# Performance work log

Hardware: AMD Instinct MI355X
Metric: run time of the kernel (lower is better)

Reference implementation:

```python
import jax, jax.numpy as jnp
import numpy as np

B, H, SQ, SK, D, INT, F = 1, 32, 2048, 2048, 128, 128, 32
THOLD = 0.5


def _mlp(x, W1, b1, W2, b2, W3, b3):
    # x: [b,h,s,d]; W*: [h,out,in] (torch Linear layout), y = x @ W^T + b, per head
    h = jax.nn.silu(jnp.einsum('bhsd,hid->bhsi', x, W1) + b1[None, :, None, :])
    h = jax.nn.silu(jnp.einsum('bhsi,hji->bhsj', h, W2) + b2[None, :, None, :])
    return jnp.einsum('bhsj,hfj->bhsf', h, W3) + b3[None, :, None, :]


def setup_inputs() -> dict:
    key = jax.random.key(0)
    ks = jax.random.split(key, 16)
    sc = 0.05  # small init so tanh stays in its linear-ish range
    inp = {
        'K': jax.random.normal(ks[0], (B, H, SK, D), jnp.float32),
        'Q': jax.random.normal(ks[1], (B, H, SQ, D), jnp.float32),
        'Wk1': jax.random.normal(ks[2], (H, INT, D), jnp.float32) * sc,
        'bk1': jax.random.normal(ks[3], (H, INT), jnp.float32) * sc,
        'Wk2': jax.random.normal(ks[4], (H, INT, INT), jnp.float32) * sc,
        'bk2': jax.random.normal(ks[5], (H, INT), jnp.float32) * sc,
        'Wk3': jax.random.normal(ks[6], (H, F, INT), jnp.float32) * sc,
        'bk3': jax.random.normal(ks[7], (H, F), jnp.float32) * sc,
        'Wq1': jax.random.normal(ks[8], (H, INT, D), jnp.float32) * sc,
        'bq1': jax.random.normal(ks[9], (H, INT), jnp.float32) * sc,
        'Wq2': jax.random.normal(ks[10], (H, INT, INT), jnp.float32) * sc,
        'bq2': jax.random.normal(ks[11], (H, INT), jnp.float32) * sc,
        'Wq3': jax.random.normal(ks[12], (H, F, INT), jnp.float32) * sc,
        'bq3': jax.random.normal(ks[13], (H, F), jnp.float32) * sc,
    }
    return inp


def reference(K, Q, Wk1, bk1, Wk2, bk2, Wk3, bk3, Wq1, bq1, Wq2, bq2, Wq3, bq3):
    # soft (hard=False) path of USA.forward
    Kl = jnp.tanh(_mlp(K, Wk1, bk1, Wk2, bk2, Wk3, bk3))  # [b,h,sk,F]
    Ql = jnp.tanh(_mlp(Q, Wq1, bq1, Wq2, bq2, Wq3, bq3))  # [b,h,sq,F]
    scores = jnp.einsum('bhtf,bhsf->bhts', Ql, Kl)        # [b,h,sq,sk]
    sq, sk = Q.shape[2], K.shape[2]
    causal = jnp.tril(jnp.ones((sq, sk), dtype=bool), k=sk - sq)
    mask_val = jnp.asarray(jnp.finfo(scores.dtype).min, scores.dtype)
    scores = jnp.where(causal[None, None], scores, mask_val)
    return jax.nn.sigmoid(scores - THOLD)
```

## Files before the change

kernel.cpp:

```cpp
#include <hip/hip_runtime.h>

#define NH  32
#define SEQ 2048
#define DIM 128
#define FD  32

typedef short          short8 __attribute__((ext_vector_type(8)));
typedef float          f32x4  __attribute__((ext_vector_type(4)));
typedef unsigned short u16x4  __attribute__((ext_vector_type(4)));

static __device__ __forceinline__ unsigned short f2bf(float f) {
    unsigned int u = __builtin_bit_cast(unsigned int, f);
    u += 0x7fffu + ((u >> 16) & 1u);
    return (unsigned short)(u >> 16);
}
static __device__ __forceinline__ float fexp(float x) {
    return __builtin_amdgcn_exp2f(x * 1.44269504088896f);
}
static __device__ __forceinline__ float sigm(float x) {
    return __builtin_amdgcn_rcpf(1.0f + fexp(-x));
}
static __device__ __forceinline__ float silu_f(float x) { return x * sigm(x); }
static __device__ __forceinline__ float tanh_f(float x) {
    return 1.0f - 2.0f * __builtin_amdgcn_rcpf(fexp(2.0f * x) + 1.0f);
}

static __device__ __forceinline__ void stage_mat(const float* __restrict__ src,
                                                 unsigned short* dst, int rows) {
    int t = threadIdx.x;
    int nit = rows >> 2;
    for (int it = 0; it < nit; ++it) {
        int row = it * 4 + (t >> 5);
        int c0  = (t & 31) * 4;
        f32x4 v = *(const f32x4*)(src + row * 128 + c0);
        u16x4 p;
        p[0] = f2bf(v[0]); p[1] = f2bf(v[1]); p[2] = f2bf(v[2]); p[3] = f2bf(v[3]);
        int base = row * 128 + (c0 ^ ((row & 7) << 3));
        *(u16x4*)(&dst[base]) = p;
    }
}

template <int OT, int ACT, bool TOGLOB>
static __device__ __forceinline__ void mlp_layer(
    unsigned short* act, const unsigned short* w_lds,
    const float* __restrict__ bias, unsigned short* __restrict__ gout) {
    int lane = threadIdx.x & 63;
    int wid  = threadIdx.x >> 6;
    int kb   = (lane >> 4) * 8;

    short8 a[2][4];
#pragma unroll
    for (int rt = 0; rt < 2; ++rt) {
        int row = wid * 32 + rt * 16 + (lane & 15);
        int sw  = (row & 7) << 3;
#pragma unroll
        for (int ks = 0; ks < 4; ++ks)
            a[rt][ks] = *(const short8*)(&act[row * 128 + ((ks * 32 + kb) ^ sw)]);
    }
    __syncthreads();
#pragma unroll
    for (int ot = 0; ot < OT; ++ot) {
        int wrow = ot * 16 + (lane & 15);
        int sw   = (wrow & 7) << 3;
        short8 b[4];
#pragma unroll
        for (int ks = 0; ks < 4; ++ks)
            b[ks] = *(const short8*)(&w_lds[wrow * 128 + ((ks * 32 + kb) ^ sw)]);
        f32x4 acc0 = {0.f, 0.f, 0.f, 0.f};
        f32x4 acc1 = {0.f, 0.f, 0.f, 0.f};
#pragma unroll
        for (int ks = 0; ks < 4; ++ks) {
            acc0 = __builtin_amdgcn_mfma_f32_16x16x32_bf16(a[0][ks], b[ks], acc0, 0, 0, 0);
            acc1 = __builtin_amdgcn_mfma_f32_16x16x32_bf16(a[1][ks], b[ks], acc1, 0, 0, 0);
        }
        float bv = bias[ot * 16 + (lane & 15)];
#pragma unroll
        for (int rt = 0; rt < 2; ++rt) {
            f32x4 acc = rt ? acc1 : acc0;
#pragma unroll
            for (int r = 0; r < 4; ++r) {
                float y = acc[r] + bv;
                float v = (ACT == 0) ? silu_f(y) : tanh_f(y);
                int orow = wid * 32 + rt * 16 + (lane >> 4) * 4 + r;
                int ocol = ot * 16 + (lane & 15);
                if (TOGLOB)
                    gout[orow * FD + ocol] = f2bf(v);
                else
                    act[orow * 128 + (ocol ^ ((orow & 7) << 3))] = f2bf(v);
            }
        }
    }
}

__global__ __launch_bounds__(128) void mlp_kernel(
    const float* __restrict__ K,  const float* __restrict__ Q,
    const float* __restrict__ Wk1, const float* __restrict__ bk1,
    const float* __restrict__ Wk2, const float* __restrict__ bk2,
    const float* __restrict__ Wk3, const float* __restrict__ bk3,
    const float* __restrict__ Wq1, const float* __restrict__ bq1,
    const float* __restrict__ Wq2, const float* __restrict__ bq2,
    const float* __restrict__ Wq3, const float* __restrict__ bq3,
    unsigned short* __restrict__ Kl, unsigned short* __restrict__ Ql) {
    __shared__ unsigned short xb[64 * 128];
    __shared__ unsigned short wb[128 * 128];
    int bid = blockIdx.x;
    int tb  = bid & 31;
    int h   = (bid >> 5) & 31;
    int src = bid >> 10;

    const float* X  = src ? Q : K;
    const float* W1 = (src ? Wq1 : Wk1) + h * (128 * 128);
    const float* B1 = (src ? bq1 : bk1) + h * 128;
    const float* W2 = (src ? Wq2 : Wk2) + h * (128 * 128);
    const float* B2 = (src ? bq2 : bk2) + h * 128;
    const float* W3 = (src ? Wq3 : Wk3) + h * (FD * 128);
    const float* B3 = (src ? bq3 : bk3) + h * FD;
    unsigned short* gout = (src ? Ql : Kl) + ((size_t)h * SEQ + (size_t)tb * 64) * FD;
    const float* xs = X + ((size_t)h * SEQ + (size_t)tb * 64) * DIM;

    stage_mat(xs, xb, 64);
    stage_mat(W1, wb, 128);
    __syncthreads();
    mlp_layer<8, 0, false>(xb, wb, B1, nullptr);
    __syncthreads();
    stage_mat(W2, wb, 128);
    __syncthreads();
    mlp_layer<8, 0, false>(xb, wb, B2, nullptr);
    __syncthreads();
    stage_mat(W3, wb, 32);
    __syncthreads();
    mlp_layer<2, 1, true>(xb, wb, B3, gout);
}

__global__ __launch_bounds__(256) void score_kernel(
    const unsigned short* __restrict__ Ql, const unsigned short* __restrict__ Kl,
    float* __restrict__ out) {
    int bid = blockIdx.x;
    int h   = bid >> 8;
    int tr  = (bid >> 4) & 15;
    int tc  = bid & 15;
    int tq0 = tr * 128, tk0 = tc * 128;
    int tid = threadIdx.x;
    float* ob = out + (size_t)h * SEQ * SEQ;

    if (tc > tr) {
        f32x4 z = {0.f, 0.f, 0.f, 0.f};
        for (int it = 0; it < 16; ++it) {
            int row = tq0 + it * 8 + (tid >> 5);
            int c0  = tk0 + (tid & 31) * 4;
            *(f32x4*)(ob + (size_t)row * SEQ + c0) = z;
        }
        return;
    }
    bool diag = (tc == tr);
    __shared__ float sb[4][32 * 68];
    int lane = tid & 63;
    int wid  = tid >> 6;
    int tqw  = tq0 + (wid >> 1) * 64;
    int tkw  = tk0 + (wid & 1) * 64;
    int kb   = (lane >> 4) * 8;

    short8 aq[4], bk[4];
#pragma unroll
    for (int i = 0; i < 4; ++i) {
        aq[i] = *(const short8*)(Ql + ((size_t)h * SEQ + tqw + i * 16 + (lane & 15)) * FD + kb);
        bk[i] = *(const short8*)(Kl + ((size_t)h * SEQ + tkw + i * 16 + (lane & 15)) * FD + kb);
    }
    float* my = sb[wid];
#pragma unroll
    for (int half = 0; half < 2; ++half) {
#pragma unroll
        for (int rt2 = 0; rt2 < 2; ++rt2) {
            int rt = half * 2 + rt2;
#pragma unroll
            for (int ct = 0; ct < 4; ++ct) {
                f32x4 acc = {0.f, 0.f, 0.f, 0.f};
                acc = __builtin_amdgcn_mfma_f32_16x16x32_bf16(aq[rt], bk[ct], acc, 0, 0, 0);
#pragma unroll
                for (int r = 0; r < 4; ++r) {
                    int row = rt2 * 16 + (lane >> 4) * 4 + r;
                    int col = ct * 16 + (lane & 15);
                    float o = sigm(acc[r] - 0.5f);
                    if (diag && (tkw + col) > (tqw + half * 32 + row)) o = 0.0f;
                    my[row * 68 + col] = o;
                }
            }
        }
#pragma unroll
        for (int it = 0; it < 4; ++it) {
            int row = it * 8 + (lane >> 3);
            int c0  = (lane & 7) * 8;
            f32x4 v0 = *(const f32x4*)(&my[row * 68 + c0]);
            f32x4 v1 = *(const f32x4*)(&my[row * 68 + c0 + 4]);
            float* dst = ob + (size_t)(tqw + half * 32 + row) * SEQ + tkw + c0;
            *(f32x4*)dst       = v0;
            *(f32x4*)(dst + 4) = v1;
        }
    }
}

extern "C" void kernel_launch(void* const* d_in, const int* in_sizes, int n_in,
                              void* d_out, int out_size, void* d_ws, size_t ws_size,
                              hipStream_t stream) {
    const float* K   = (const float*)d_in[0];
    const float* Q   = (const float*)d_in[1];
    const float* Wk1 = (const float*)d_in[2];
    const float* bk1 = (const float*)d_in[3];
    const float* Wk2 = (const float*)d_in[4];
    const float* bk2 = (const float*)d_in[5];
    const float* Wk3 = (const float*)d_in[6];
    const float* bk3 = (const float*)d_in[7];
    const float* Wq1 = (const float*)d_in[8];
    const float* bq1 = (const float*)d_in[9];
    const float* Wq2 = (const float*)d_in[10];
    const float* bq2 = (const float*)d_in[11];
    const float* Wq3 = (const float*)d_in[12];
    const float* bq3 = (const float*)d_in[13];

    unsigned short* Kl = (unsigned short*)d_ws;
    unsigned short* Ql = Kl + (size_t)NH * SEQ * FD;

    mlp_kernel<<<dim3(2 * NH * (SEQ / 64)), dim3(128), 0, stream>>>(
        K, Q, Wk1, bk1, Wk2, bk2, Wk3, bk3, Wq1, bq1, Wq2, bq2, Wq3, bq3, Kl, Ql);

    score_kernel<<<dim3(NH * 16 * 16), dim3(256), 0, stream>>>(
        Ql, Kl, (float*)d_out);
}
```

Baseline: 173.6 us.

## Pre-convert MLP weights to bf16 once and read them directly from global memory

Adds a prep kernel that converts all MLP weights to a packed bf16 image in the workspace. The MLP kernel then reads weight fragments straight from global/L2 instead of staging them in LDS, loads the input tile directly into registers, and reorders block indices so blocks of the same head share cached weights. Layer 3 output is staged in LDS and written with vector stores, and the score kernel uses nontemporal stores for its large output. This removes repeated per-block fp32-to-bf16 weight conversion and LDS staging barriers, at the cost of an extra launch and more global weight traffic per block.

```diff
diff --git a/kernel.cpp b/kernel.cpp
--- a/kernel.cpp
+++ b/kernel.cpp
@@ -8,6 +8,7 @@
 typedef short          short8 __attribute__((ext_vector_type(8)));
 typedef float          f32x4  __attribute__((ext_vector_type(4)));
 typedef unsigned short u16x4  __attribute__((ext_vector_type(4)));
+typedef unsigned short u16x8  __attribute__((ext_vector_type(8)));
 
 static __device__ __forceinline__ unsigned short f2bf(float f) {
     unsigned int u = __builtin_bit_cast(unsigned int, f);
@@ -24,48 +25,72 @@
 static __device__ __forceinline__ float tanh_f(float x) {
     return 1.0f - 2.0f * __builtin_amdgcn_rcpf(fexp(2.0f * x) + 1.0f);
 }
-
-static __device__ __forceinline__ void stage_mat(const float* __restrict__ src,
-                                                 unsigned short* dst, int rows) {
-    int t = threadIdx.x;
-    int nit = rows >> 2;
-    for (int it = 0; it < nit; ++it) {
-        int row = it * 4 + (t >> 5);
-        int c0  = (t & 31) * 4;
-        f32x4 v = *(const f32x4*)(src + row * 128 + c0);
-        u16x4 p;
-        p[0] = f2bf(v[0]); p[1] = f2bf(v[1]); p[2] = f2bf(v[2]); p[3] = f2bf(v[3]);
-        int base = row * 128 + (c0 ^ ((row & 7) << 3));
-        *(u16x4*)(&dst[base]) = p;
-    }
-}
-
-template <int OT, int ACT, bool TOGLOB>
-static __device__ __forceinline__ void mlp_layer(
-    unsigned short* act, const unsigned short* w_lds,
-    const float* __restrict__ bias, unsigned short* __restrict__ gout) {
-    int lane = threadIdx.x & 63;
-    int wid  = threadIdx.x >> 6;
-    int kb   = (lane >> 4) * 8;
-
-    short8 a[2][4];
+static __device__ __forceinline__ void ntst(float* p, f32x4 v) {
+    __builtin_nontemporal_store(v, (f32x4*)p);
+}
+
+#define WIMG_PER_HEAD 36864
+#define WIMG_PER_SRC  (32 * WIMG_PER_HEAD)
+
+__global__ __launch_bounds__(256) void prep_weights(
+    const float* __restrict__ Wk1, const float* __restrict__ Wk2,
+    const float* __restrict__ Wk3, const float* __restrict__ Wq1,
+    const float* __restrict__ Wq2, const float* __restrict__ Wq3,
+    unsigned short* __restrict__ wimg) {
+    int c = blockIdx.x * 256 + threadIdx.x;
+    int s = (c >= 147456) ? 1 : 0;
+    c -= s * 147456;
+    const float* src;
+    int dst;
+    int sB = s * WIMG_PER_SRC;
+    if (c < 65536) {
+        int h = c >> 11, j = (c & 2047) * 8;
+        src = (s ? Wq1 : Wk1) + h * 16384 + j;
+        dst = sB + h * WIMG_PER_HEAD + j;
+    } else if (c < 131072) {
+        int cc = c - 65536;
+        int h = cc >> 11, j = (cc & 2047) * 8;
+        src = (s ? Wq2 : Wk2) + h * 16384 + j;
+        dst = sB + h * WIMG_PER_HEAD + 16384 + j;
+    } else {
+        int cc = c - 131072;
+        int h = cc >> 9, j = (cc & 511) * 8;
+        src = (s ? Wq3 : Wk3) + h * 4096 + j;
+        dst = sB + h * WIMG_PER_HEAD + 32768 + j;
+    }
+    f32x4 u0 = *(const f32x4*)src;
+    f32x4 u1 = *(const f32x4*)(src + 4);
+    u16x8 p;
+    p[0] = f2bf(u0[0]); p[1] = f2bf(u0[1]); p[2] = f2bf(u0[2]); p[3] = f2bf(u0[3]);
+    p[4] = f2bf(u1[0]); p[5] = f2bf(u1[1]); p[6] = f2bf(u1[2]); p[7] = f2bf(u1[3]);
+    *(u16x8*)(&wimg[dst]) = p;
+}
+
+static __device__ __forceinline__ void loadA_lds(const unsigned short* act,
+                                                 short8 a[2][4], int lane, int wid) {
+    int r0 = lane & 15, kb = (lane >> 4) * 8;
 #pragma unroll
     for (int rt = 0; rt < 2; ++rt) {
-        int row = wid * 32 + rt * 16 + (lane & 15);
+        int row = wid * 32 + rt * 16 + r0;
         int sw  = (row & 7) << 3;
 #pragma unroll
         for (int ks = 0; ks < 4; ++ks)
             a[rt][ks] = *(const short8*)(&act[row * 128 + ((ks * 32 + kb) ^ sw)]);
     }
-    __syncthreads();
+}
+
+template <int OT, int ACT, bool LIN>
+static __device__ __forceinline__ void compute_store(
+    const short8 a[2][4], const unsigned short* __restrict__ W,
+    const float* __restrict__ bias, unsigned short* act, int lane, int wid) {
+    int r0 = lane & 15, kb = (lane >> 4) * 8;
 #pragma unroll
     for (int ot = 0; ot < OT; ++ot) {
-        int wrow = ot * 16 + (lane & 15);
-        int sw   = (wrow & 7) << 3;
+        int wrow = ot * 16 + r0;
         short8 b[4];
 #pragma unroll
         for (int ks = 0; ks < 4; ++ks)
-            b[ks] = *(const short8*)(&w_lds[wrow * 128 + ((ks * 32 + kb) ^ sw)]);
+            b[ks] = *(const short8*)(W + wrow * 128 + ks * 32 + kb);
         f32x4 acc0 = {0.f, 0.f, 0.f, 0.f};
         f32x4 acc1 = {0.f, 0.f, 0.f, 0.f};
 #pragma unroll
@@ -73,7 +98,7 @@
             acc0 = __builtin_amdgcn_mfma_f32_16x16x32_bf16(a[0][ks], b[ks], acc0, 0, 0, 0);
             acc1 = __builtin_amdgcn_mfma_f32_16x16x32_bf16(a[1][ks], b[ks], acc1, 0, 0, 0);
         }
-        float bv = bias[ot * 16 + (lane & 15)];
+        float bv = bias[wrow];
 #pragma unroll
         for (int rt = 0; rt < 2; ++rt) {
             f32x4 acc = rt ? acc1 : acc0;
@@ -82,9 +107,9 @@
                 float y = acc[r] + bv;
                 float v = (ACT == 0) ? silu_f(y) : tanh_f(y);
                 int orow = wid * 32 + rt * 16 + (lane >> 4) * 4 + r;
-                int ocol = ot * 16 + (lane & 15);
-                if (TOGLOB)
-                    gout[orow * FD + ocol] = f2bf(v);
+                int ocol = ot * 16 + r0;
+                if (LIN)
+                    act[orow * FD + ocol] = f2bf(v);
                 else
                     act[orow * 128 + (ocol ^ ((orow & 7) << 3))] = f2bf(v);
             }
@@ -94,42 +119,56 @@
 
 __global__ __launch_bounds__(128) void mlp_kernel(
     const float* __restrict__ K,  const float* __restrict__ Q,
-    const float* __restrict__ Wk1, const float* __restrict__ bk1,
-    const float* __restrict__ Wk2, const float* __restrict__ bk2,
-    const float* __restrict__ Wk3, const float* __restrict__ bk3,
-    const float* __restrict__ Wq1, const float* __restrict__ bq1,
-    const float* __restrict__ Wq2, const float* __restrict__ bq2,
-    const float* __restrict__ Wq3, const float* __restrict__ bq3,
+    const float* __restrict__ bk1, const float* __restrict__ bk2,
+    const float* __restrict__ bk3, const float* __restrict__ bq1,
+    const float* __restrict__ bq2, const float* __restrict__ bq3,
+    const unsigned short* __restrict__ wimg,
     unsigned short* __restrict__ Kl, unsigned short* __restrict__ Ql) {
-    __shared__ unsigned short xb[64 * 128];
-    __shared__ unsigned short wb[128 * 128];
-    int bid = blockIdx.x;
+    __shared__ unsigned short act[64 * 128];
+    int raw = blockIdx.x;
+    int bid = (raw & 7) * 256 + (raw >> 3);
     int tb  = bid & 31;
     int h   = (bid >> 5) & 31;
-    int src = bid >> 10;
-
-    const float* X  = src ? Q : K;
-    const float* W1 = (src ? Wq1 : Wk1) + h * (128 * 128);
-    const float* B1 = (src ? bq1 : bk1) + h * 128;
-    const float* W2 = (src ? Wq2 : Wk2) + h * (128 * 128);
-    const float* B2 = (src ? bq2 : bk2) + h * 128;
-    const float* W3 = (src ? Wq3 : Wk3) + h * (FD * 128);
-    const float* B3 = (src ? bq3 : bk3) + h * FD;
-    unsigned short* gout = (src ? Ql : Kl) + ((size_t)h * SEQ + (size_t)tb * 64) * FD;
+    int s   = bid >> 10;
+
+    const float* X  = s ? Q : K;
+    const unsigned short* Wb = wimg + s * WIMG_PER_SRC + h * WIMG_PER_HEAD;
+    const float* B1 = (s ? bq1 : bk1) + h * 128;
+    const float* B2 = (s ? bq2 : bk2) + h * 128;
+    const float* B3 = (s ? bq3 : bk3) + h * FD;
+    unsigned short* gout = (s ? Ql : Kl) + ((size_t)h * SEQ + (size_t)tb * 64) * FD;
+
+    int lane = threadIdx.x & 63, wid = threadIdx.x >> 6;
+    int r0 = lane & 15, kb = (lane >> 4) * 8;
+
+    short8 a[2][4];
     const float* xs = X + ((size_t)h * SEQ + (size_t)tb * 64) * DIM;
-
-    stage_mat(xs, xb, 64);
-    stage_mat(W1, wb, 128);
+#pragma unroll
+    for (int rt = 0; rt < 2; ++rt) {
+        int row = wid * 32 + rt * 16 + r0;
+#pragma unroll
+        for (int ks = 0; ks < 4; ++ks) {
+            const float* p = xs + row * 128 + ks * 32 + kb;
+            f32x4 u0 = *(const f32x4*)p;
+            f32x4 u1 = *(const f32x4*)(p + 4);
+            short8 t;
+            t[0] = f2bf(u0[0]); t[1] = f2bf(u0[1]); t[2] = f2bf(u0[2]); t[3] = f2bf(u0[3]);
+            t[4] = f2bf(u1[0]); t[5] = f2bf(u1[1]); t[6] = f2bf(u1[2]); t[7] = f2bf(u1[3]);
+            a[rt][ks] = t;
+        }
+    }
+    compute_store<8, 0, false>(a, Wb, B1, act, lane, wid);
+    loadA_lds(act, a, lane, wid);
+    compute_store<8, 0, false>(a, Wb + 16384, B2, act, lane, wid);
+    loadA_lds(act, a, lane, wid);
     __syncthreads();
-    mlp_layer<8, 0, false>(xb, wb, B1, nullptr);
+    compute_store<2, 1, true>(a, Wb + 32768, B3, act, lane, wid);
     __syncthreads();
-    stage_mat(W2, wb, 128);
-    __syncthreads();
-    mlp_layer<8, 0, false>(xb, wb, B2, nullptr);
-    __syncthreads();
-    stage_mat(W3, wb, 32);
-    __syncthreads();
-    mlp_layer<2, 1, true>(xb, wb, B3, gout);
+    int t = threadIdx.x;
+    u16x8 v0 = *(const u16x8*)(&act[t * 16]);
+    u16x8 v1 = *(const u16x8*)(&act[t * 16 + 8]);
+    *(u16x8*)(gout + t * 16)     = v0;
+    *(u16x8*)(gout + t * 16 + 8) = v1;
 }
 
 __global__ __launch_bounds__(256) void score_kernel(
@@ -148,7 +187,7 @@
         for (int it = 0; it < 16; ++it) {
             int row = tq0 + it * 8 + (tid >> 5);
             int c0  = tk0 + (tid & 31) * 4;
-            *(f32x4*)(ob + (size_t)row * SEQ + c0) = z;
+            ntst(ob + (size_t)row * SEQ + c0, z);
         }
         return;
     }
@@ -193,8 +232,8 @@
             f32x4 v0 = *(const f32x4*)(&my[row * 68 + c0]);
             f32x4 v1 = *(const f32x4*)(&my[row * 68 + c0 + 4]);
             float* dst = ob + (size_t)(tqw + half * 32 + row) * SEQ + tkw + c0;
-            *(f32x4*)dst       = v0;
-            *(f32x4*)(dst + 4) = v1;
+            ntst(dst,     v0);
+            ntst(dst + 4, v1);
         }
     }
 }
@@ -217,11 +256,15 @@
     const float* Wq3 = (const float*)d_in[12];
     const float* bq3 = (const float*)d_in[13];
 
-    unsigned short* Kl = (unsigned short*)d_ws;
-    unsigned short* Ql = Kl + (size_t)NH * SEQ * FD;
+    unsigned short* Kl   = (unsigned short*)d_ws;
+    unsigned short* Ql   = Kl + (size_t)NH * SEQ * FD;
+    unsigned short* wimg = Ql + (size_t)NH * SEQ * FD;
+
+    prep_weights<<<dim3(1152), dim3(256), 0, stream>>>(
+        Wk1, Wk2, Wk3, Wq1, Wq2, Wq3, wimg);
 
     mlp_kernel<<<dim3(2 * NH * (SEQ / 64)), dim3(128), 0, stream>>>(
-        K, Q, Wk1, bk1, Wk2, bk2, Wk3, bk3, Wq1, bq1, Wq2, bq2, Wq3, bq3, Kl, Ql);
+        K, Q, bk1, bk2, bk3, bq1, bq2, bq3, wimg, Kl, Ql);
 
     score_kernel<<<dim3(NH * 16 * 16), dim3(256), 0, stream>>>(
         Ql, Kl, (float*)d_out);
```

After: 265.1 us. 1.53x slower.
